# Kernel optimization log

Measured on AMD Instinct MI355X. Metric: run time of the kernel, lower is better.

Reference implementation:

```python
import jax, jax.numpy as jnp
import numpy as np

N = 50000      # nodes
E = 800000     # edges
IN = 128       # in_dim
EMB = 32       # emb_dim
ED = 8         # edge_dim
L = 4          # num_layers
B = 64         # num graphs in batch
OUT = 10       # out_dim
EPS = 1e-5


def setup_inputs() -> dict:
    key = jax.random.key(0)
    ks = jax.random.split(key, 16)
    f32 = jnp.float32
    def nrm(k, shape, scale):
        return jax.random.normal(k, shape, dtype=f32) * scale
    inp = {}
    inp['x'] = nrm(ks[0], (N, IN), 1.0)
    inp['edge_index'] = jax.random.randint(ks[1], (2, E), 0, N)
    inp['edge_attr'] = nrm(ks[2], (E, ED), 1.0)
    inp['batch'] = jnp.sort(jax.random.randint(ks[3], (N,), 0, B))
    # lin_in
    inp['lin_in_w'] = nrm(ks[4], (IN, EMB), 0.05)
    inp['lin_in_b'] = jnp.zeros((EMB,), f32)
    # per-layer message MLP: Linear(2e+ed->e), BN, ReLU, Linear(e->e), BN, ReLU
    inp['msg_w1'] = nrm(ks[5], (L, 2 * EMB + ED, EMB), 0.1)
    inp['msg_b1'] = jnp.zeros((L, EMB), f32)
    inp['msg_g1'] = jnp.ones((L, EMB), f32)
    inp['msg_be1'] = jnp.zeros((L, EMB), f32)
    inp['msg_w2'] = nrm(ks[6], (L, EMB, EMB), 0.1)
    inp['msg_b2'] = jnp.zeros((L, EMB), f32)
    inp['msg_g2'] = jnp.ones((L, EMB), f32)
    inp['msg_be2'] = jnp.zeros((L, EMB), f32)
    # per-layer update MLP: Linear(2e->e), BN, ReLU, Linear(e->e), BN, ReLU
    inp['upd_w1'] = nrm(ks[7], (L, 2 * EMB, EMB), 0.1)
    inp['upd_b1'] = jnp.zeros((L, EMB), f32)
    inp['upd_g1'] = jnp.ones((L, EMB), f32)
    inp['upd_be1'] = jnp.zeros((L, EMB), f32)
    inp['upd_w2'] = nrm(ks[8], (L, EMB, EMB), 0.1)
    inp['upd_b2'] = jnp.zeros((L, EMB), f32)
    inp['upd_g2'] = jnp.ones((L, EMB), f32)
    inp['upd_be2'] = jnp.zeros((L, EMB), f32)
    # lin_pred
    inp['pred_w'] = nrm(ks[9], (EMB, OUT), 0.1)
    inp['pred_b'] = jnp.zeros((OUT,), f32)
    return inp


def _bn(x, g, b):
    # BatchNorm1d in training mode: batch stats over dim 0 (biased variance)
    mu = jnp.mean(x, axis=0)
    var = jnp.mean(jnp.square(x - mu), axis=0)
    return (x - mu) * jax.lax.rsqrt(var + EPS) * g + b


def reference(x, edge_attr, lin_in_w, lin_in_b,
              msg_w1, msg_b1, msg_g1, msg_be1, msg_w2, msg_b2, msg_g2, msg_be2,
              upd_w1, upd_b1, upd_g1, upd_be1, upd_w2, upd_b2, upd_g2, upd_be2,
              pred_w, pred_b, edge_index, batch):
    src = edge_index[0]  # h_j source nodes
    dst = edge_index[1]  # h_i target nodes (aggregation index)
    h = x @ lin_in_w + lin_in_b  # [N, EMB]
    for i in range(L):
        # message: gather + concat + MLP(BN,ReLU)x2 over edges
        msg_in = jnp.concatenate([h[dst], h[src], edge_attr], axis=-1)  # [E, 2e+ed]
        m = jax.nn.relu(_bn(msg_in @ msg_w1[i] + msg_b1[i], msg_g1[i], msg_be1[i]))
        m = jax.nn.relu(_bn(m @ msg_w2[i] + msg_b2[i], msg_g2[i], msg_be2[i]))
        # aggregate: scatter-add by destination
        aggr = jax.ops.segment_sum(m, dst, num_segments=N)  # [N, EMB]
        # update: concat + MLP(BN,ReLU)x2
        u = jnp.concatenate([h, aggr], axis=-1)  # [N, 2e]
        u = jax.nn.relu(_bn(u @ upd_w1[i] + upd_b1[i], upd_g1[i], upd_be1[i]))
        u = jax.nn.relu(_bn(u @ upd_w2[i] + upd_b2[i], upd_g2[i], upd_be2[i]))
        h = u + h  # residual in MPNNModel.get_embeddings
    # global mean pool
    sums = jax.ops.segment_sum(h, batch, num_segments=B)
    counts = jax.ops.segment_sum(jnp.ones((N,), h.dtype), batch, num_segments=B)
    h_graph = sums / jnp.maximum(counts, 1.0)[:, None]
    return h_graph @ pred_w + pred_b  # [B, OUT]
```

## Files before the change

### kernel.cpp

```cpp
#include <hip/hip_runtime.h>
#include <cstddef>

#define N_NODES 50000
#define N_EDGES 800000
#define IN_DIM  128
#define EMB     32
#define ED      8
#define NLAYERS 4
#define NB      64
#define OUTD    10
#define EPS_BN  1e-5f

#define EDGE_GRID 3125
#define NODE_GRID 196
#define NODE4_GRID 782
#define AU_GRID   6250
#define NTILE_N   3125
#define LIN_GRID  782
#define ST_TPW    4
#define ST_GRID   3125
#define MSG2_TPW  4
#define MSG2_GRID 3125

#define SREP 4

typedef short bf16x8 __attribute__((ext_vector_type(8)));
typedef float f32x4  __attribute__((ext_vector_type(4)));


__device__ __forceinline__ unsigned short f2bf(float x) {
  union { float f; unsigned u; } v; v.f = x;
  unsigned b = v.u + 0x7FFFu + ((v.u >> 16) & 1u);
  return (unsigned short)(b >> 16);
}
__device__ __forceinline__ float bf2f(unsigned short s) {
  union { unsigned u; float f; } v; v.u = ((unsigned)s) << 16;
  return v.f;
}

__device__ __forceinline__ void coef_from_stats(const float* __restrict__ stats_stage,
                                                const float* __restrict__ g,
                                                const float* __restrict__ be,
                                                float inv_count, float* __restrict__ cf) {
  if (threadIdx.x < EMB) {
    const int c = threadIdx.x;
    float s = 0.f, ss = 0.f;
#pragma unroll
    for (int r = 0; r < SREP; ++r) {
      s  += stats_stage[r*64 + c];
      ss += stats_stage[r*64 + EMB + c];
    }
    const float mu  = s * inv_count;
    const float var = ss * inv_count - mu*mu;
    const float a = g[c] * rsqrtf(var + EPS_BN);
    cf[c] = a;
    cf[EMB + c] = fmaf(-mu, a, be[c]);
  }
  __syncthreads();
}

__device__ __forceinline__ void wave_stats_atomic(float ts[8], float tss[8],
                                                  float* __restrict__ lds_s,
                                                  float* __restrict__ lds_q,
                                                  float* __restrict__ stats_stage) {
  const int lane = threadIdx.x & 63;
  const int wv   = threadIdx.x >> 6;
#pragma unroll
  for (int j = 0; j < 8; ++j) {
    float a = ts[j], b = tss[j];
#pragma unroll
    for (int o = 32; o > 0; o >>= 1) {
      a += __shfl_down(a, o, 64);
      b += __shfl_down(b, o, 64);
    }
    ts[j] = a; tss[j] = b;
  }
  if (lane == 0) {
#pragma unroll
    for (int j = 0; j < 8; ++j) {
      lds_s[wv*8 + j] = ts[j];
      lds_q[wv*8 + j] = tss[j];
    }
  }
  __syncthreads();
  if (threadIdx.x < 64) {
    const float v = (threadIdx.x < 32) ? lds_s[threadIdx.x] : lds_q[threadIdx.x - 32];
    atomicAdd(stats_stage + ((blockIdx.x & (SREP-1)) << 6) + threadIdx.x, v);
  }
}

#define HSTRIDE 40

__global__ __launch_bounds__(256) void k_lin_in_pq(
    const float* __restrict__ x, const float* __restrict__ w, const float* __restrict__ b,
    const float* __restrict__ w1, const float* __restrict__ b1, const int* __restrict__ ei,
    float* __restrict__ h, unsigned short* __restrict__ p, unsigned short* __restrict__ q,
    int* __restrict__ cnt)
{
  __shared__ __align__(16) unsigned short lds_hb[4][16*HSTRIDE];
  __shared__ __align__(16) unsigned short lds_pq[4][16*HSTRIDE];
  const int lane = threadIdx.x & 63;
  const int wv   = threadIdx.x >> 6;
  const int n0i  = lane & 15;
  const int quad = lane >> 4;

  const int tile = blockIdx.x*4 + wv;
  if (tile < NTILE_N) {
    const int r0 = tile*16;
    bf16x8 BwL[4], BwH[4];
#pragma unroll
    for (int kb = 0; kb < 4; ++kb) {
#pragma unroll
      for (int j = 0; j < 8; ++j) {
        const int k = kb*32 + quad*8 + j;
        BwL[kb][j] = (short)f2bf(w[k*EMB + n0i]);
        BwH[kb][j] = (short)f2bf(w[k*EMB + 16 + n0i]);
      }
    }
    f32x4 accL = {0.f,0.f,0.f,0.f};
    f32x4 accH = {0.f,0.f,0.f,0.f};
#pragma unroll
    for (int kb = 0; kb < 4; ++kb) {
      const float4 xa = *(const float4*)(x + (size_t)(r0 + n0i)*IN_DIM + kb*32 + quad*8);
      const float4 xb = *(const float4*)(x + (size_t)(r0 + n0i)*IN_DIM + kb*32 + quad*8 + 4);
      bf16x8 A;
      A[0] = (short)f2bf(xa.x); A[1] = (short)f2bf(xa.y);
      A[2] = (short)f2bf(xa.z); A[3] = (short)f2bf(xa.w);
      A[4] = (short)f2bf(xb.x); A[5] = (short)f2bf(xb.y);
      A[6] = (short)f2bf(xb.z); A[7] = (short)f2bf(xb.w);
      accL = __builtin_amdgcn_mfma_f32_16x16x32_bf16(A, BwL[kb], accL, 0, 0, 0);
      accH = __builtin_amdgcn_mfma_f32_16x16x32_bf16(A, BwH[kb], accH, 0, 0, 0);
    }
    const float bL = b[n0i], bH = b[16 + n0i];
#pragma unroll
    for (int r = 0; r < 4; ++r) {
      const int row = quad*4 + r;
      const float vL = accL[r] + bL;
      const float vH = accH[r] + bH;
      h[(size_t)(r0 + row)*EMB + n0i]      = vL;
      h[(size_t)(r0 + row)*EMB + 16 + n0i] = vH;
      lds_hb[wv][row*HSTRIDE + n0i]      = f2bf(vL);
      lds_hb[wv][row*HSTRIDE + 16 + n0i] = f2bf(vH);
    }
    bf16x8 A2;
#pragma unroll
    for (int j = 0; j < 8; ++j)
      A2[j] = (short)lds_hb[wv][n0i*HSTRIDE + quad*8 + j];
    bf16x8 BpL, BpH, BqL, BqH;
#pragma unroll
    for (int j = 0; j < 8; ++j) {
      const int k = quad*8 + j;
      BpL[j] = (short)f2bf(w1[k*EMB + n0i]);
      BpH[j] = (short)f2bf(w1[k*EMB + 16 + n0i]);
      BqL[j] = (short)f2bf(w1[(EMB + k)*EMB + n0i]);
      BqH[j] = (short)f2bf(w1[(EMB + k)*EMB + 16 + n0i]);
    }
    const f32x4 z4 = {0.f,0.f,0.f,0.f};
    f32x4 pL = __builtin_amdgcn_mfma_f32_16x16x32_bf16(A2, BpL, z4, 0, 0, 0);
    f32x4 pH = __builtin_amdgcn_mfma_f32_16x16x32_bf16(A2, BpH, z4, 0, 0, 0);
    f32x4 qL = __builtin_amdgcn_mfma_f32_16x16x32_bf16(A2, BqL, z4, 0, 0, 0);
    f32x4 qH = __builtin_amdgcn_mfma_f32_16x16x32_bf16(A2, BqH, z4, 0, 0, 0);
    const float b1L = b1[n0i], b1H = b1[16 + n0i];
#pragma unroll
    for (int r = 0; r < 4; ++r) {
      const int row = quad*4 + r;
      lds_pq[wv][row*HSTRIDE + n0i]      = f2bf(pL[r] + b1L);
      lds_pq[wv][row*HSTRIDE + 16 + n0i] = f2bf(pH[r] + b1H);
    }
    {
      const int row2 = lane >> 2;
      const int c8   = (lane & 3)*8;
      const uint4 ov = *(const uint4*)&lds_pq[wv][row2*HSTRIDE + c8];
      *(uint4*)(p + (size_t)(r0 + row2)*EMB + c8) = ov;
    }
#pragma unroll
    for (int r = 0; r < 4; ++r) {
      const int row = quad*4 + r;
      lds_pq[wv][row*HSTRIDE + n0i]      = f2bf(qL[r]);
      lds_pq[wv][row*HSTRIDE + 16 + n0i] = f2bf(qH[r]);
    }
    {
      const int row2 = lane >> 2;
      const int c8   = (lane & 3)*8;
      const uint4 ov = *(const uint4*)&lds_pq[wv][row2*HSTRIDE + c8];
      *(uint4*)(q + (size_t)(r0 + row2)*EMB + c8) = ov;
    }
  }
  for (int e = blockIdx.x*256 + threadIdx.x; e < N_EDGES; e += gridDim.x*256)
    atomicAdd(&cnt[ei[N_EDGES + e]], 1);
}

__global__ __launch_bounds__(256) void k_scan_a(const int* __restrict__ cnt,
                                                int* __restrict__ row_ptr, int* __restrict__ bsum) {
  __shared__ int s[256];
  const int gid = blockIdx.x*256 + threadIdx.x;
  const int v = (gid < N_NODES) ? cnt[gid] : 0;
  s[threadIdx.x] = v;
  __syncthreads();
  for (int o = 1; o < 256; o <<= 1) {
    const int t = (threadIdx.x >= o) ? s[threadIdx.x - o] : 0;
    __syncthreads();
    s[threadIdx.x] += t;
    __syncthreads();
  }
  if (gid < N_NODES) row_ptr[gid] = s[threadIdx.x] - v;
  if (threadIdx.x == 255) bsum[blockIdx.x] = s[255];
}

__global__ __launch_bounds__(256) void k_scan_bc(int* __restrict__ row_ptr,
                                                 const int* __restrict__ bsum) {
  __shared__ int s[256];
  const int t = threadIdx.x;
  const int v = (t < NODE_GRID) ? bsum[t] : 0;
  s[t] = v;
  __syncthreads();
  for (int o = 1; o < 256; o <<= 1) {
    const int tt = (t >= o) ? s[t - o] : 0;
    __syncthreads();
    s[t] += tt;
    __syncthreads();
  }
  const int off = (blockIdx.x == 0) ? 0 : s[blockIdx.x - 1];
  const int gid = blockIdx.x*256 + t;
  if (gid < N_NODES) row_ptr[gid] += off;
  if (blockIdx.x == 0 && t == 0) row_ptr[N_NODES] = N_EDGES;
}

__global__ __launch_bounds__(256) void k_place_scatter(
    const int* __restrict__ ei, const float* __restrict__ ea,
    const int* __restrict__ row_ptr, int* __restrict__ cnt2,
    uint2* __restrict__ rec)
{
  const int e = blockIdx.x*256 + threadIdx.x;
  const int s = ei[e];
  const int d = ei[N_EDGES + e];
  const int pos = row_ptr[d] + atomicAdd(&cnt2[d], 1);
  const float4 v0 = ((const float4*)(ea + (size_t)e*ED))[0];
  const float4 v1 = ((const float4*)(ea + (size_t)e*ED))[1];
  const float ev[8] = {v0.x, v0.y, v0.z, v0.w, v1.x, v1.y, v1.z, v1.w};
  unsigned u[4];
#pragma unroll
  for (int j = 0; j < 4; ++j)
    u[j] = (unsigned)f2bf(ev[2*j]) | ((unsigned)f2bf(ev[2*j+1]) << 16);
  uint2* rp = rec + (size_t)pos*3;
  rp[0] = make_uint2((unsigned)s, (unsigned)d);
  rp[1] = make_uint2(u[0], u[1]);
  rp[2] = make_uint2(u[2], u[3]);
}


__global__ __launch_bounds__(256) void k_stats1(
    const unsigned short* __restrict__ pb, const unsigned short* __restrict__ qb,
    const uint2* __restrict__ rec, const float* __restrict__ w1b,
    float* __restrict__ stats)
{
  __shared__ float lds_d[4][16*33];
  __shared__ float lds_s[4][32], lds_q[4][32];
  const int lane = threadIdx.x & 63;
  const int wv   = threadIdx.x >> 6;
  const int l15  = lane & 15;
  const int quad = lane >> 4;

  bf16x8 B1lo = {}, B1hi = {};
  if (quad == 0) {
#pragma unroll
    for (int j = 0; j < 8; ++j) {
      B1lo[j] = (short)f2bf(w1b[j*EMB + l15]);
      B1hi[j] = (short)f2bf(w1b[j*EMB + 16 + l15]);
    }
  }

  float ts[8], tss[8];
#pragma unroll
  for (int j = 0; j < 8; ++j) { ts[j] = 0.f; tss[j] = 0.f; }

  const int tile0 = blockIdx.x * (4*ST_TPW);
#pragma unroll
  for (int t = 0; t < ST_TPW; ++t) {
    const int tile = tile0 + t*4 + wv;
    const size_t e0 = (size_t)tile * 16;

    bf16x8 A = {};
    if (quad == 0) {
      const uint2 rb = rec[(e0 + l15)*3 + 1];
      const uint2 rc = rec[(e0 + l15)*3 + 2];
      A[0] = (short)(rb.x & 0xFFFFu); A[1] = (short)(rb.x >> 16);
      A[2] = (short)(rb.y & 0xFFFFu); A[3] = (short)(rb.y >> 16);
      A[4] = (short)(rc.x & 0xFFFFu); A[5] = (short)(rc.x >> 16);
      A[6] = (short)(rc.y & 0xFFFFu); A[7] = (short)(rc.y >> 16);
    }
    const f32x4 z4 = {0.f,0.f,0.f,0.f};
    f32x4 D0 = __builtin_amdgcn_mfma_f32_16x16x32_bf16(A, B1lo, z4, 0, 0, 0);
    f32x4 D1 = __builtin_amdgcn_mfma_f32_16x16x32_bf16(A, B1hi, z4, 0, 0, 0);
#pragma unroll
    for (int r = 0; r < 4; ++r) {
      const int row = quad*4 + r;
      lds_d[wv][row*33 + l15]      = D0[r];
      lds_d[wv][row*33 + 16 + l15] = D1[r];
    }
    const uint2 sd = rec[(e0 + l15)*3];
    const uint4 pg = *(const uint4*)(pb + (size_t)sd.y*EMB + quad*8);
    const uint4 qg = *(const uint4*)(qb + (size_t)sd.x*EMB + quad*8);
    const unsigned pu[4] = {pg.x, pg.y, pg.z, pg.w};
    const unsigned qu[4] = {qg.x, qg.y, qg.z, qg.w};
#pragma unroll
    for (int jj = 0; jj < 4; ++jj) {
      const float d0 = lds_d[wv][l15*33 + quad*8 + 2*jj];
      const float d1 = lds_d[wv][l15*33 + quad*8 + 2*jj + 1];
      const float v0 = (d0 + bf2f((unsigned short)(pu[jj] & 0xFFFFu)))
                            + bf2f((unsigned short)(qu[jj] & 0xFFFFu));
      const float v1 = (d1 + bf2f((unsigned short)(pu[jj] >> 16)))
                            + bf2f((unsigned short)(qu[jj] >> 16));
      const float w0 = bf2f(f2bf(v0));
      const float w1v = bf2f(f2bf(v1));
      ts[2*jj]   += w0;  tss[2*jj]   = fmaf(w0, w0, tss[2*jj]);
      ts[2*jj+1] += w1v; tss[2*jj+1] = fmaf(w1v, w1v, tss[2*jj+1]);
    }
  }

#pragma unroll
  for (int j = 0; j < 8; ++j) {
    float a = ts[j], b = tss[j];
#pragma unroll
    for (int o = 1; o < 16; o <<= 1) {
      a += __shfl_xor(a, o, 64);
      b += __shfl_xor(b, o, 64);
    }
    ts[j] = a; tss[j] = b;
  }
  if (l15 == 0) {
#pragma unroll
    for (int j = 0; j < 8; ++j) {
      lds_s[wv][quad*8 + j] = ts[j];
      lds_q[wv][quad*8 + j] = tss[j];
    }
  }
  __syncthreads();
  if (threadIdx.x < 64) {
    const int c = threadIdx.x & 31;
    const int kind = threadIdx.x >> 5;
    float v = 0.f;
#pragma unroll
    for (int wq = 0; wq < 4; ++wq)
      v += kind ? lds_q[wq][c] : lds_s[wq][c];
    atomicAdd(stats + ((blockIdx.x & (SREP-1)) << 6) + kind*32 + c, v);
  }
}

__global__ __launch_bounds__(256) void k_msg2(
    const unsigned short* __restrict__ pb, const unsigned short* __restrict__ qb,
    const uint2* __restrict__ rec, const float* __restrict__ w1b,
    const float* __restrict__ stats1, const float* __restrict__ g1, const float* __restrict__ be1,
    const float* __restrict__ w2, const float* __restrict__ b2,
    unsigned short* __restrict__ y, float* __restrict__ stats2)
{
  __shared__ float lds_d[4][16*33];
  __shared__ __align__(16) unsigned short lds_t[4][16*32];
  __shared__ float lds_s[4][32], lds_q[4][32];
  __shared__ float cf[64];

  coef_from_stats(stats1, g1, be1, 1.0f/(float)N_EDGES, cf);

  const int lane = threadIdx.x & 63;
  const int wv   = threadIdx.x >> 6;
  const int l15  = lane & 15;
  const int quad = lane >> 4;

  bf16x8 B1lo = {}, B1hi = {};
  if (quad == 0) {
#pragma unroll
    for (int j = 0; j < 8; ++j) {
      B1lo[j] = (short)f2bf(w1b[j*EMB + l15]);
      B1hi[j] = (short)f2bf(w1b[j*EMB + 16 + l15]);
    }
  }
  bf16x8 Blo, Bhi;
#pragma unroll
  for (int j = 0; j < 8; ++j) {
    Blo[j] = (short)f2bf(w2[(quad*8 + j)*EMB + l15]);
    Bhi[j] = (short)f2bf(w2[(quad*8 + j)*EMB + 16 + l15]);
  }
  float a1[8], c1[8];
#pragma unroll
  for (int j = 0; j < 8; ++j) {
    a1[j] = cf[quad*8 + j];
    c1[j] = cf[EMB + quad*8 + j];
  }
  const float b2c0 = b2[l15], b2c1 = b2[16 + l15];

  float ts[8], tss[8];
#pragma unroll
  for (int j = 0; j < 8; ++j) { ts[j] = 0.f; tss[j] = 0.f; }

  const int tile0 = blockIdx.x * (4*MSG2_TPW);
#pragma unroll
  for (int t = 0; t < MSG2_TPW; ++t) {
    const int tile = tile0 + t*4 + wv;
    const size_t e0 = (size_t)tile * 16;

    bf16x8 A = {};
    if (quad == 0) {
      const uint2 rb = rec[(e0 + l15)*3 + 1];
      const uint2 rc = rec[(e0 + l15)*3 + 2];
      A[0] = (short)(rb.x & 0xFFFFu); A[1] = (short)(rb.x >> 16);
      A[2] = (short)(rb.y & 0xFFFFu); A[3] = (short)(rb.y >> 16);
      A[4] = (short)(rc.x & 0xFFFFu); A[5] = (short)(rc.x >> 16);
      A[6] = (short)(rc.y & 0xFFFFu); A[7] = (short)(rc.y >> 16);
    }
    const f32x4 z4 = {0.f,0.f,0.f,0.f};
    f32x4 D0 = __builtin_amdgcn_mfma_f32_16x16x32_bf16(A, B1lo, z4, 0, 0, 0);
    f32x4 D1 = __builtin_amdgcn_mfma_f32_16x16x32_bf16(A, B1hi, z4, 0, 0, 0);
#pragma unroll
    for (int r = 0; r < 4; ++r) {
      const int row = quad*4 + r;
      lds_d[wv][row*33 + l15]      = D0[r];
      lds_d[wv][row*33 + 16 + l15] = D1[r];
    }
    const uint2 sd = rec[(e0 + l15)*3];
    const uint4 pg = *(const uint4*)(pb + (size_t)sd.y*EMB + quad*8);
    const uint4 qg = *(const uint4*)(qb + (size_t)sd.x*EMB + quad*8);
    const unsigned pu[4] = {pg.x, pg.y, pg.z, pg.w};
    const unsigned qu[4] = {qg.x, qg.y, qg.z, qg.w};
    bf16x8 A2;
#pragma unroll
    for (int jj = 0; jj < 4; ++jj) {
      const float d0 = lds_d[wv][l15*33 + quad*8 + 2*jj];
      const float d1 = lds_d[wv][l15*33 + quad*8 + 2*jj + 1];
      const float v0 = (d0 + bf2f((unsigned short)(pu[jj] & 0xFFFFu)))
                            + bf2f((unsigned short)(qu[jj] & 0xFFFFu));
      const float v1 = (d1 + bf2f((unsigned short)(pu[jj] >> 16)))
                            + bf2f((unsigned short)(qu[jj] >> 16));
      const float w0 = bf2f(f2bf(v0));
      const float w1v = bf2f(f2bf(v1));
      const float r0 = fmaxf(fmaf(a1[2*jj],   w0,  c1[2*jj]),   0.f);
      const float r1 = fmaxf(fmaf(a1[2*jj+1], w1v, c1[2*jj+1]), 0.f);
      A2[2*jj]   = (short)f2bf(r0);
      A2[2*jj+1] = (short)f2bf(r1);
    }

    f32x4 acc0 = {0.f, 0.f, 0.f, 0.f};
    f32x4 acc1 = {0.f, 0.f, 0.f, 0.f};
    acc0 = __builtin_amdgcn_mfma_f32_16x16x32_bf16(A2, Blo, acc0, 0, 0, 0);
    acc1 = __builtin_amdgcn_mfma_f32_16x16x32_bf16(A2, Bhi, acc1, 0, 0, 0);

#pragma unroll
    for (int r = 0; r < 4; ++r) {
      const int row = quad*4 + r;
      lds_t[wv][row*32 + l15]      = f2bf(acc0[r] + b2c0);
      lds_t[wv][row*32 + 16 + l15] = f2bf(acc1[r] + b2c1);
    }
    const uint4 orow = *(const uint4*)&lds_t[wv][(lane>>2)*32 + (lane&3)*8];
    *(uint4*)(y + (e0 + (lane>>2))*EMB + (lane&3)*8) = orow;

    const unsigned uo[4] = {orow.x, orow.y, orow.z, orow.w};
#pragma unroll
    for (int j = 0; j < 4; ++j) {
      const float v0 = bf2f((unsigned short)(uo[j] & 0xFFFFu));
      const float v1 = bf2f((unsigned short)(uo[j] >> 16));
      ts[2*j]   += v0;  tss[2*j]   = fmaf(v0, v0, tss[2*j]);
      ts[2*j+1] += v1;  tss[2*j+1] = fmaf(v1, v1, tss[2*j+1]);
    }
  }

#pragma unroll
  for (int j = 0; j < 8; ++j) {
    float s = ts[j], qq = tss[j];
#pragma unroll
    for (int o = 4; o < 64; o <<= 1) {
      s  += __shfl_xor(s, o, 64);
      qq += __shfl_xor(qq, o, 64);
    }
    ts[j] = s; tss[j] = qq;
  }
  if (lane < 4) {
#pragma unroll
    for (int j = 0; j < 8; ++j) {
      lds_s[wv][lane*8 + j] = ts[j];
      lds_q[wv][lane*8 + j] = tss[j];
    }
  }
  __syncthreads();
  if (threadIdx.x < 64) {
    const int c = threadIdx.x & 31;
    const int kind = threadIdx.x >> 5;
    float v = 0.f;
#pragma unroll
    for (int wq = 0; wq < 4; ++wq)
      v += kind ? lds_q[wq][c] : lds_s[wq][c];
    atomicAdd(stats2 + ((blockIdx.x & (SREP-1)) << 6) + kind*32 + c, v);
  }
}

__global__ __launch_bounds__(256) void k_aggr_upd1(
    const unsigned short* __restrict__ y, const int* __restrict__ row_ptr,
    const float* __restrict__ h,
    const float* __restrict__ stats1, const float* __restrict__ g2, const float* __restrict__ be2,
    const float* __restrict__ uw1, const float* __restrict__ ub1,
    float* __restrict__ z, float* __restrict__ stats2)
{
  __shared__ float cf[64];
  __shared__ float lh[8][32];
  __shared__ float la[8][32];
  __shared__ float rs[4][32], rq[4][32];
  coef_from_stats(stats1, g2, be2, 1.0f/(float)N_EDGES, cf);

  const int g = threadIdx.x >> 5;
  const int l = threadIdx.x & 31;
  const int n = blockIdx.x*8 + g;

  lh[g][l] = h[(size_t)n*EMB + l];

  const int rof = l >> 4;
  const int cp  = l & 15;
  const float a0 = cf[2*cp],     b0 = cf[EMB + 2*cp];
  const float a1 = cf[2*cp + 1], b1 = cf[EMB + 2*cp + 1];
  const int lo = row_ptr[n], hi = row_ptr[n+1];
  float s0 = 0.f, s1 = 0.f;
  for (int i = lo + rof; i < hi; i += 2) {
    const unsigned u = *(const unsigned*)(y + (size_t)i*EMB + 2*cp);
    const float v0 = bf2f((unsigned short)(u & 0xFFFFu));
    const float v1 = bf2f((unsigned short)(u >> 16));
    s0 += fmaxf(fmaf(a0, v0, b0), 0.f);
    s1 += fmaxf(fmaf(a1, v1, b1), 0.f);
  }
  s0 += __shfl_xor(s0, 16, 64);
  s1 += __shfl_xor(s1, 16, 64);
  if (rof == 0) { la[g][2*cp] = s0; la[g][2*cp + 1] = s1; }
  __syncthreads();

  float acc = ub1[l];
#pragma unroll
  for (int k = 0; k < EMB; ++k) acc = fmaf(lh[g][k], uw1[k*EMB + l], acc);
#pragma unroll
  for (int k = 0; k < EMB; ++k) acc = fmaf(la[g][k], uw1[(EMB + k)*EMB + l], acc);
  z[(size_t)n*EMB + l] = acc;

  const float sq = acc*acc;
  const float a2 = acc + __shfl_down(acc, 32, 64);
  const float q2 = sq  + __shfl_down(sq,  32, 64);
  const int wv = threadIdx.x >> 6;
  if ((threadIdx.x & 63) < 32) { rs[wv][l] = a2; rq[wv][l] = q2; }
  __syncthreads();
  if (threadIdx.x < 64) {
    const int c = threadIdx.x & 31;
    const int kind = threadIdx.x >> 5;
    float v = 0.f;
#pragma unroll
    for (int wq = 0; wq < 4; ++wq)
      v += kind ? rq[wq][c] : rs[wq][c];
    atomicAdd(stats2 + ((blockIdx.x & (SREP-1)) << 6) + kind*32 + c, v);
  }
}

__global__ __launch_bounds__(256) void k_upd2(
    float* __restrict__ z,
    const float* __restrict__ stats1, const float* __restrict__ g1, const float* __restrict__ be1,
    const float* __restrict__ w, const float* __restrict__ b,
    float* __restrict__ stats2)
{
  __shared__ float cf[64];
  __shared__ float lds_s[32], lds_q[32];
  coef_from_stats(stats1, g1, be1, 1.0f/(float)N_NODES, cf);

  const int lane = threadIdx.x & 63;
  const int wv   = threadIdx.x >> 6;
  const int n  = blockIdx.x*64 + lane;
  const int c0 = wv*8;
  float acc[8];
#pragma unroll
  for (int j = 0; j < 8; ++j) acc[j] = 0.f;
  if (n < N_NODES) {
#pragma unroll
    for (int j = 0; j < 8; ++j) acc[j] = b[c0 + j];
    const float4* zp = (const float4*)(z + (size_t)n*EMB);
#pragma unroll
    for (int k4 = 0; k4 < 8; ++k4) {
      const float4 v = zp[k4];
      const float mv[4] = {v.x, v.y, v.z, v.w};
#pragma unroll
      for (int t = 0; t < 4; ++t) {
        const int k = 4*k4 + t;
        const float m = fmaxf(fmaf(cf[k], mv[t], cf[EMB + k]), 0.f);
        const float* wk = w + k*EMB + c0;
#pragma unroll
        for (int j = 0; j < 8; ++j) acc[j] = fmaf(m, wk[j], acc[j]);
      }
    }
  }
  float ts[8], tss[8];
#pragma unroll
  for (int j = 0; j < 8; ++j) { ts[j] = acc[j]; tss[j] = acc[j]*acc[j]; }
  wave_stats_atomic(ts, tss, lds_s, lds_q, stats2);
  if (n < N_NODES) {
    float4 o0, o1;
    o0.x = acc[0]; o0.y = acc[1]; o0.z = acc[2]; o0.w = acc[3];
    o1.x = acc[4]; o1.y = acc[5]; o1.z = acc[6]; o1.w = acc[7];
    *(float4*)(z + (size_t)n*EMB + c0)     = o0;
    *(float4*)(z + (size_t)n*EMB + c0 + 4) = o1;
  }
}

__global__ __launch_bounds__(256) void k_resid_pq(
    float* __restrict__ h, const float* __restrict__ z,
    const float* __restrict__ stats, const float* __restrict__ g, const float* __restrict__ be,
    const float* __restrict__ w1_next, const float* __restrict__ b1_next,
    unsigned short* __restrict__ p, unsigned short* __restrict__ q)
{
  __shared__ float cf[64];
  __shared__ float lds_h[64][33];
  coef_from_stats(stats, g, be, 1.0f/(float)N_NODES, cf);

  const int lane = threadIdx.x & 63;
  const int wv   = threadIdx.x >> 6;
  const int n  = blockIdx.x*64 + lane;
  const int c0 = wv*8;
  if (n < N_NODES) {
    const float4* zp = (const float4*)(z + (size_t)n*EMB + c0);
    float4* hp = (float4*)(h + (size_t)n*EMB + c0);
    float hn[8];
    const float4 z0 = zp[0], z1 = zp[1];
    const float4 h0 = hp[0], h1 = hp[1];
    const float zv[8] = {z0.x, z0.y, z0.z, z0.w, z1.x, z1.y, z1.z, z1.w};
    const float hv[8] = {h0.x, h0.y, h0.z, h0.w, h1.x, h1.y, h1.z, h1.w};
#pragma unroll
    for (int j = 0; j < 8; ++j) {
      const int k = c0 + j;
      hn[j] = hv[j] + fmaxf(fmaf(cf[k], zv[j], cf[EMB + k]), 0.f);
      lds_h[lane][k] = hn[j];
    }
    float4 o0, o1;
    o0.x = hn[0]; o0.y = hn[1]; o0.z = hn[2]; o0.w = hn[3];
    o1.x = hn[4]; o1.y = hn[5]; o1.z = hn[6]; o1.w = hn[7];
    hp[0] = o0; hp[1] = o1;
  }
  __syncthreads();
  if (n < N_NODES && w1_next) {
    float ap[8], aq[8];
#pragma unroll
    for (int j = 0; j < 8; ++j) { ap[j] = b1_next[c0 + j]; aq[j] = 0.f; }
#pragma unroll
    for (int k = 0; k < EMB; ++k) {
      const float hvv = lds_h[lane][k];
      const float* wp = w1_next + k*EMB + c0;
      const float* wq = w1_next + (EMB + k)*EMB + c0;
#pragma unroll
      for (int j = 0; j < 8; ++j) ap[j] = fmaf(hvv, wp[j], ap[j]);
#pragma unroll
      for (int j = 0; j < 8; ++j) aq[j] = fmaf(hvv, wq[j], aq[j]);
    }
    unsigned up[4], uq[4];
#pragma unroll
    for (int j = 0; j < 4; ++j) {
      up[j] = (unsigned)f2bf(ap[2*j]) | ((unsigned)f2bf(ap[2*j+1]) << 16);
      uq[j] = (unsigned)f2bf(aq[2*j]) | ((unsigned)f2bf(aq[2*j+1]) << 16);
    }
    uint4 op; op.x = up[0]; op.y = up[1]; op.z = up[2]; op.w = up[3];
    uint4 oq; oq.x = uq[0]; oq.y = uq[1]; oq.z = uq[2]; oq.w = uq[3];
    *(uint4*)(p + (size_t)n*EMB + c0) = op;
    *(uint4*)(q + (size_t)n*EMB + c0) = oq;
  }
}

__global__ void k_pool(const float* __restrict__ h, const int* __restrict__ batch,
                       const float* __restrict__ pw, const float* __restrict__ pb,
                       float* __restrict__ out)
{
  __shared__ float sred[256];
  __shared__ float hg[EMB];
  const int b = blockIdx.x;
  int lo = 0, hi = N_NODES;
  while (lo < hi) { int m = (lo + hi) >> 1; if (batch[m] < b) lo = m + 1; else hi = m; }
  const int start = lo;
  hi = N_NODES;
  while (lo < hi) { int m = (lo + hi) >> 1; if (batch[m] < b + 1) lo = m + 1; else hi = m; }
  const int end = lo;

  const int c = threadIdx.x & (EMB-1);
  const int r = threadIdx.x >> 5;
  float s = 0.f;
  for (int n = start + r; n < end; n += 8) s += h[(size_t)n*EMB + c];
  sred[threadIdx.x] = s;
  __syncthreads();
  if (threadIdx.x < EMB) {
    float tot = 0.f;
#pragma unroll
    for (int r2 = 0; r2 < 8; ++r2) tot += sred[r2*EMB + threadIdx.x];
    const float cnt = (float)(end - start);
    hg[threadIdx.x] = tot / fmaxf(cnt, 1.f);
  }
  __syncthreads();
  if (threadIdx.x < OUTD) {
    float acc = pb[threadIdx.x];
#pragma unroll
    for (int cc = 0; cc < EMB; ++cc) acc = fmaf(hg[cc], pw[cc*OUTD + threadIdx.x], acc);
    out[b*OUTD + threadIdx.x] = acc;
  }
}


extern "C" void kernel_launch(void* const* d_in, const int* in_sizes, int n_in,
                              void* d_out, int out_size, void* d_ws, size_t ws_size,
                              hipStream_t stream) {
  const float* x        = (const float*)d_in[0];
  const int*   ei       = (const int*)  d_in[1];
  const float* ea       = (const float*)d_in[2];
  const int*   batch    = (const int*)  d_in[3];
  const float* lin_in_w = (const float*)d_in[4];
  const float* lin_in_b = (const float*)d_in[5];
  const float* msg_w1   = (const float*)d_in[6];
  const float* msg_b1   = (const float*)d_in[7];
  const float* msg_g1   = (const float*)d_in[8];
  const float* msg_be1  = (const float*)d_in[9];
  const float* msg_w2   = (const float*)d_in[10];
  const float* msg_b2   = (const float*)d_in[11];
  const float* msg_g2   = (const float*)d_in[12];
  const float* msg_be2  = (const float*)d_in[13];
  const float* upd_w1   = (const float*)d_in[14];
  const float* upd_b1   = (const float*)d_in[15];
  const float* upd_g1   = (const float*)d_in[16];
  const float* upd_be1  = (const float*)d_in[17];
  const float* upd_w2   = (const float*)d_in[18];
  const float* upd_b2   = (const float*)d_in[19];
  const float* upd_g2   = (const float*)d_in[20];
  const float* upd_be2  = (const float*)d_in[21];
  const float* pred_w   = (const float*)d_in[22];
  const float* pred_b   = (const float*)d_in[23];
  float* out = (float*)d_out;

  char* wsb = (char*)d_ws;
  unsigned short* y  = (unsigned short*)wsb;
  uint2* rec = (uint2*)(wsb + (size_t)N_EDGES*EMB*2);
  unsigned short* p  = (unsigned short*)(rec + (size_t)N_EDGES*3);
  unsigned short* q  = p + (size_t)N_NODES*EMB;
  float* h       = (float*)(q + (size_t)N_NODES*EMB);
  float* z       = h + (size_t)N_NODES*EMB;
  float* stats   = z + (size_t)N_NODES*EMB;
  int*   cnt     = (int*)(stats + 16*SREP*64);
  int*   cnt2    = cnt + N_NODES;
  int*   row_ptr = cnt2 + N_NODES;
  int*   bsum    = row_ptr + N_NODES + 1;
  const size_t need = ((size_t)((char*)(bsum + 256) - wsb));
  if (ws_size < need) return;

  hipMemsetAsync(stats, 0, (16*SREP*64 + 2*N_NODES)*sizeof(float), stream);

  k_lin_in_pq<<<LIN_GRID, 256, 0, stream>>>(x, lin_in_w, lin_in_b, msg_w1, msg_b1, ei,
                                            h, p, q, cnt);
  k_scan_a<<<NODE_GRID, 256, 0, stream>>>(cnt, row_ptr, bsum);
  k_scan_bc<<<NODE_GRID, 256, 0, stream>>>(row_ptr, bsum);
  k_place_scatter<<<EDGE_GRID, 256, 0, stream>>>(ei, ea, row_ptr, cnt2, rec);

  for (int l = 0; l < NLAYERS; ++l) {
    const int st = l*4;
    const float* w1  = msg_w1 + (size_t)l*(2*EMB+ED)*EMB;
    const float* w1b = w1 + (size_t)2*EMB*EMB;
    const float* w2  = msg_w2 + (size_t)l*EMB*EMB;
    const float* uw1 = upd_w1 + (size_t)l*(2*EMB)*EMB;
    const float* uw2 = upd_w2 + (size_t)l*EMB*EMB;
    const float* w1_next = (l+1 < NLAYERS) ? msg_w1 + (size_t)(l+1)*(2*EMB+ED)*EMB : nullptr;
    const float* b1_next = (l+1 < NLAYERS) ? msg_b1 + (size_t)(l+1)*EMB : nullptr;

    k_stats1<<<ST_GRID, 256, 0, stream>>>(p, q, rec, w1b, stats + (size_t)st*SREP*64);
    k_msg2<<<MSG2_GRID, 256, 0, stream>>>(p, q, rec, w1b,
                                          stats + (size_t)st*SREP*64,
                                          msg_g1 + l*EMB, msg_be1 + l*EMB,
                                          w2, msg_b2 + l*EMB,
                                          y, stats + (size_t)(st+1)*SREP*64);
    k_aggr_upd1<<<AU_GRID, 256, 0, stream>>>(y, row_ptr, h,
                                             stats + (size_t)(st+1)*SREP*64,
                                             msg_g2 + l*EMB, msg_be2 + l*EMB,
                                             uw1, upd_b1 + l*EMB,
                                             z, stats + (size_t)(st+2)*SREP*64);
    k_upd2<<<NODE4_GRID, 256, 0, stream>>>(z, stats + (size_t)(st+2)*SREP*64,
                                           upd_g1 + l*EMB, upd_be1 + l*EMB,
                                           uw2, upd_b2 + l*EMB, stats + (size_t)(st+3)*SREP*64);
    k_resid_pq<<<NODE4_GRID, 256, 0, stream>>>(h, z, stats + (size_t)(st+3)*SREP*64,
                                               upd_g2 + l*EMB, upd_be2 + l*EMB,
                                               w1_next, b1_next, p, q);
  }

  k_pool<<<NB, 256, 0, stream>>>(h, batch, pred_w, pred_b, out);
}
```

Measured before the change: 847.8 us.

## Pad edge records to 32 bytes and prefetch gathers across tiles

Edge records are widened from three 8-byte words to two 16-byte vectors, so src, dst and the first half of the edge attributes arrive in one 16-byte load. k_stats1 now issues all record loads and node-row gathers for its tiles before any compute. k_msg2 software-pipelines the next tile's record and gather loads during the current tile's compute. This targets latency-bound dependent gathers, at the cost of extra registers and a larger record buffer (padding raises it from 24 to 32 bytes per edge).

```diff
diff --git a/kernel.cpp b/kernel.cpp
--- a/kernel.cpp
+++ b/kernel.cpp
@@ -229,7 +229,7 @@
 __global__ __launch_bounds__(256) void k_place_scatter(
     const int* __restrict__ ei, const float* __restrict__ ea,
     const int* __restrict__ row_ptr, int* __restrict__ cnt2,
-    uint2* __restrict__ rec)
+    uint4* __restrict__ rec)
 {
   const int e = blockIdx.x*256 + threadIdx.x;
   const int s = ei[e];
@@ -242,16 +242,15 @@
 #pragma unroll
   for (int j = 0; j < 4; ++j)
     u[j] = (unsigned)f2bf(ev[2*j]) | ((unsigned)f2bf(ev[2*j+1]) << 16);
-  uint2* rp = rec + (size_t)pos*3;
-  rp[0] = make_uint2((unsigned)s, (unsigned)d);
-  rp[1] = make_uint2(u[0], u[1]);
-  rp[2] = make_uint2(u[2], u[3]);
+  uint4* rp = rec + (size_t)pos*2;
+  rp[0] = make_uint4((unsigned)s, (unsigned)d, u[0], u[1]);
+  rp[1] = make_uint4(u[2], u[3], 0u, 0u);
 }
 
 
 __global__ __launch_bounds__(256) void k_stats1(
     const unsigned short* __restrict__ pb, const unsigned short* __restrict__ qb,
-    const uint2* __restrict__ rec, const float* __restrict__ w1b,
+    const uint4* __restrict__ rec, const float* __restrict__ w1b,
     float* __restrict__ stats)
 {
   __shared__ float lds_d[4][16*33];
@@ -270,24 +269,35 @@
     }
   }
 
-  float ts[8], tss[8];
-#pragma unroll
-  for (int j = 0; j < 8; ++j) { ts[j] = 0.f; tss[j] = 0.f; }
-
   const int tile0 = blockIdx.x * (4*ST_TPW);
+  uint4 RA[ST_TPW], RB[ST_TPW];
 #pragma unroll
   for (int t = 0; t < ST_TPW; ++t) {
     const int tile = tile0 + t*4 + wv;
     const size_t e0 = (size_t)tile * 16;
-
+    const uint4* r4 = rec + (e0 + l15)*2;
+    RA[t] = r4[0];
+    RB[t] = (quad == 0) ? r4[1] : make_uint4(0u,0u,0u,0u);
+  }
+  uint4 PG[ST_TPW], QG[ST_TPW];
+#pragma unroll
+  for (int t = 0; t < ST_TPW; ++t) {
+    PG[t] = *(const uint4*)(pb + (size_t)RA[t].y*EMB + quad*8);
+    QG[t] = *(const uint4*)(qb + (size_t)RA[t].x*EMB + quad*8);
+  }
+
+  float ts[8], tss[8];
+#pragma unroll
+  for (int j = 0; j < 8; ++j) { ts[j] = 0.f; tss[j] = 0.f; }
+
+#pragma unroll
+  for (int t = 0; t < ST_TPW; ++t) {
     bf16x8 A = {};
     if (quad == 0) {
-      const uint2 rb = rec[(e0 + l15)*3 + 1];
-      const uint2 rc = rec[(e0 + l15)*3 + 2];
-      A[0] = (short)(rb.x & 0xFFFFu); A[1] = (short)(rb.x >> 16);
-      A[2] = (short)(rb.y & 0xFFFFu); A[3] = (short)(rb.y >> 16);
-      A[4] = (short)(rc.x & 0xFFFFu); A[5] = (short)(rc.x >> 16);
-      A[6] = (short)(rc.y & 0xFFFFu); A[7] = (short)(rc.y >> 16);
+      A[0] = (short)(RA[t].z & 0xFFFFu); A[1] = (short)(RA[t].z >> 16);
+      A[2] = (short)(RA[t].w & 0xFFFFu); A[3] = (short)(RA[t].w >> 16);
+      A[4] = (short)(RB[t].x & 0xFFFFu); A[5] = (short)(RB[t].x >> 16);
+      A[6] = (short)(RB[t].y & 0xFFFFu); A[7] = (short)(RB[t].y >> 16);
     }
     const f32x4 z4 = {0.f,0.f,0.f,0.f};
     f32x4 D0 = __builtin_amdgcn_mfma_f32_16x16x32_bf16(A, B1lo, z4, 0, 0, 0);
@@ -298,11 +308,8 @@
       lds_d[wv][row*33 + l15]      = D0[r];
       lds_d[wv][row*33 + 16 + l15] = D1[r];
     }
-    const uint2 sd = rec[(e0 + l15)*3];
-    const uint4 pg = *(const uint4*)(pb + (size_t)sd.y*EMB + quad*8);
-    const uint4 qg = *(const uint4*)(qb + (size_t)sd.x*EMB + quad*8);
-    const unsigned pu[4] = {pg.x, pg.y, pg.z, pg.w};
-    const unsigned qu[4] = {qg.x, qg.y, qg.z, qg.w};
+    const unsigned pu[4] = {PG[t].x, PG[t].y, PG[t].z, PG[t].w};
+    const unsigned qu[4] = {QG[t].x, QG[t].y, QG[t].z, QG[t].w};
 #pragma unroll
     for (int jj = 0; jj < 4; ++jj) {
       const float d0 = lds_d[wv][l15*33 + quad*8 + 2*jj];
@@ -349,7 +356,7 @@
 
 __global__ __launch_bounds__(256) void k_msg2(
     const unsigned short* __restrict__ pb, const unsigned short* __restrict__ qb,
-    const uint2* __restrict__ rec, const float* __restrict__ w1b,
+    const uint4* __restrict__ rec, const float* __restrict__ w1b,
     const float* __restrict__ stats1, const float* __restrict__ g1, const float* __restrict__ be1,
     const float* __restrict__ w2, const float* __restrict__ b2,
     unsigned short* __restrict__ y, float* __restrict__ stats2)
@@ -393,19 +400,36 @@
   for (int j = 0; j < 8; ++j) { ts[j] = 0.f; tss[j] = 0.f; }
 
   const int tile0 = blockIdx.x * (4*MSG2_TPW);
+
+  uint4 cRA, cRB, cPG, cQG;
+  {
+    const size_t e0 = (size_t)(tile0 + wv) * 16;
+    const uint4* r4 = rec + (e0 + l15)*2;
+    cRA = r4[0];
+    cRB = (quad == 0) ? r4[1] : make_uint4(0u,0u,0u,0u);
+    cPG = *(const uint4*)(pb + (size_t)cRA.y*EMB + quad*8);
+    cQG = *(const uint4*)(qb + (size_t)cRA.x*EMB + quad*8);
+  }
+
 #pragma unroll
   for (int t = 0; t < MSG2_TPW; ++t) {
-    const int tile = tile0 + t*4 + wv;
-    const size_t e0 = (size_t)tile * 16;
+    const size_t e0 = (size_t)(tile0 + t*4 + wv) * 16;
+
+    uint4 nRA = make_uint4(0u,0u,0u,0u), nRB = make_uint4(0u,0u,0u,0u);
+    uint4 nPG = make_uint4(0u,0u,0u,0u), nQG = make_uint4(0u,0u,0u,0u);
+    if (t + 1 < MSG2_TPW) {
+      const size_t e1 = (size_t)(tile0 + (t+1)*4 + wv) * 16;
+      const uint4* r4 = rec + (e1 + l15)*2;
+      nRA = r4[0];
+      nRB = (quad == 0) ? r4[1] : make_uint4(0u,0u,0u,0u);
+    }
 
     bf16x8 A = {};
     if (quad == 0) {
-      const uint2 rb = rec[(e0 + l15)*3 + 1];
-      const uint2 rc = rec[(e0 + l15)*3 + 2];
-      A[0] = (short)(rb.x & 0xFFFFu); A[1] = (short)(rb.x >> 16);
-      A[2] = (short)(rb.y & 0xFFFFu); A[3] = (short)(rb.y >> 16);
-      A[4] = (short)(rc.x & 0xFFFFu); A[5] = (short)(rc.x >> 16);
-      A[6] = (short)(rc.y & 0xFFFFu); A[7] = (short)(rc.y >> 16);
+      A[0] = (short)(cRA.z & 0xFFFFu); A[1] = (short)(cRA.z >> 16);
+      A[2] = (short)(cRA.w & 0xFFFFu); A[3] = (short)(cRA.w >> 16);
+      A[4] = (short)(cRB.x & 0xFFFFu); A[5] = (short)(cRB.x >> 16);
+      A[6] = (short)(cRB.y & 0xFFFFu); A[7] = (short)(cRB.y >> 16);
     }
     const f32x4 z4 = {0.f,0.f,0.f,0.f};
     f32x4 D0 = __builtin_amdgcn_mfma_f32_16x16x32_bf16(A, B1lo, z4, 0, 0, 0);
@@ -416,11 +440,14 @@
       lds_d[wv][row*33 + l15]      = D0[r];
       lds_d[wv][row*33 + 16 + l15] = D1[r];
     }
-    const uint2 sd = rec[(e0 + l15)*3];
-    const uint4 pg = *(const uint4*)(pb + (size_t)sd.y*EMB + quad*8);
-    const uint4 qg = *(const uint4*)(qb + (size_t)sd.x*EMB + quad*8);
-    const unsigned pu[4] = {pg.x, pg.y, pg.z, pg.w};
-    const unsigned qu[4] = {qg.x, qg.y, qg.z, qg.w};
+
+    if (t + 1 < MSG2_TPW) {
+      nPG = *(const uint4*)(pb + (size_t)nRA.y*EMB + quad*8);
+      nQG = *(const uint4*)(qb + (size_t)nRA.x*EMB + quad*8);
+    }
+
+    const unsigned pu[4] = {cPG.x, cPG.y, cPG.z, cPG.w};
+    const unsigned qu[4] = {cQG.x, cQG.y, cQG.z, cQG.w};
     bf16x8 A2;
 #pragma unroll
     for (int jj = 0; jj < 4; ++jj) {
@@ -460,6 +487,8 @@
       ts[2*j]   += v0;  tss[2*j]   = fmaf(v0, v0, tss[2*j]);
       ts[2*j+1] += v1;  tss[2*j+1] = fmaf(v1, v1, tss[2*j+1]);
     }
+
+    cRA = nRA; cRB = nRB; cPG = nPG; cQG = nQG;
   }
 
 #pragma unroll
@@ -729,8 +758,8 @@
 
   char* wsb = (char*)d_ws;
   unsigned short* y  = (unsigned short*)wsb;
-  uint2* rec = (uint2*)(wsb + (size_t)N_EDGES*EMB*2);
-  unsigned short* p  = (unsigned short*)(rec + (size_t)N_EDGES*3);
+  uint4* rec = (uint4*)(wsb + (size_t)N_EDGES*EMB*2);
+  unsigned short* p  = (unsigned short*)(rec + (size_t)N_EDGES*2);
   unsigned short* q  = p + (size_t)N_NODES*EMB;
   float* h       = (float*)(q + (size_t)N_NODES*EMB);
   float* z       = h + (size_t)N_NODES*EMB;
```

Result: faster. 826.5 us (-2.5%).
